# Kernel tuning notes

Hardware: AMD Instinct MI355X
Metric: run time of the kernel (lower is better)

Reference implementation:

```python
import jax, jax.numpy as jnp
import numpy as np

HIDDEN = 512
ONEHOT = 64
B, L = 128, 1024


def setup_inputs() -> dict:
    key = jax.random.key(0)
    k1, k2, k3, k4, k5 = jax.random.split(key, 5)
    hidden = jax.random.normal(k1, (B, HIDDEN), dtype=jnp.float32)
    encoder_outputs = jax.random.normal(k2, (L, B, HIDDEN + ONEHOT), dtype=jnp.float32)
    # nn.Linear(2*hidden+onehot, hidden): weight (out, in), bias (out,)
    fan_in = 2 * HIDDEN + ONEHOT
    bound = 1.0 / np.sqrt(fan_in)
    W = jax.random.uniform(k3, (HIDDEN, fan_in), minval=-bound, maxval=bound, dtype=jnp.float32)
    b = jax.random.uniform(k4, (HIDDEN,), minval=-bound, maxval=bound, dtype=jnp.float32)
    stdv = 1.0 / np.sqrt(HIDDEN)
    v = jax.random.normal(k5, (HIDDEN,), dtype=jnp.float32) * stdv
    return {"hidden": hidden, "encoder_outputs": encoder_outputs, "W": W, "b": b, "v": v}


def reference(hidden, encoder_outputs, W, b, v):
    # hidden: (B, H), encoder_outputs: (L, B, H+onehot)
    h_dim = hidden.shape[1]
    enc = jnp.transpose(encoder_outputs, (1, 0, 2))  # (B, L, H+onehot)
    # Split the linear into two partial matmuls to avoid the explicit repeat+concat:
    # attn(cat([H_rep, enc])) == hidden @ Wh.T (broadcast over L) + enc @ We.T + b
    Wh = W[:, :h_dim]          # (H, H)
    We = W[:, h_dim:]          # (H, H+onehot)
    part_h = hidden @ Wh.T      # (B, H)
    part_e = jnp.einsum('bld,hd->blh', enc, We)  # (B, L, H)
    energy = jnp.tanh(part_e + part_h[:, None, :] + b)  # (B, L, H)
    scores = jnp.einsum('blh,h->bl', energy, v)          # (B, L)
    return jax.nn.softmax(scores, axis=1)[:, None, :]    # (B, 1, L)
```

## Files before the change

### kernel.cpp

```cpp
#include <hip/hip_runtime.h>
#include <stdint.h>

#define HIDDEN 512
#define ONEHOT 64
#define EDIM   576
#define BATCH  128
#define LSEQ   1024
#define FANIN  1088

typedef __attribute__((ext_vector_type(8))) short short8;
typedef __attribute__((ext_vector_type(4))) float f32x4;

__device__ inline unsigned short f2bf(float x) {
    union { float f; unsigned int u; } v; v.f = x;
    unsigned int u = v.u;
    unsigned int r = (u + 0x7FFFu + ((u >> 16) & 1u)) >> 16;
    return (unsigned short)r;
}

__device__ inline float fast_tanh(float x) {
    float ax = fabsf(x);
    float e  = __expf(2.f * ax);
    float t  = 1.f - __fdividef(2.f, e + 1.f);
    return copysignf(t, x);
}

__global__ __launch_bounds__(256) void k_prep(const float* __restrict__ hidden,
                                              const float* __restrict__ W,
                                              const float* __restrict__ bias,
                                              float* __restrict__ ph,
                                              unsigned short* __restrict__ WeB) {
    int bid = blockIdx.x;
    int tid = threadIdx.x;
    if (bid < 256) {
        int gid = bid * 256 + tid;
        int b = gid & (BATCH - 1);
        int h = gid >> 7;
        const float* hrow = hidden + b * HIDDEN;
        const float* wrow = W + h * FANIN;
        float acc = 0.f;
#pragma unroll 4
        for (int d = 0; d < HIDDEN; d += 4) {
            float4 hv = *(const float4*)(hrow + d);
            float4 wv = *(const float4*)(wrow + d);
            acc += hv.x * wv.x + hv.y * wv.y + hv.z * wv.z + hv.w * wv.w;
        }
        ph[b * HIDDEN + h] = acc + bias[h];
    } else {
        int i = (bid - 256) * 256 + tid;
        int kc = i >> 15;
        int h  = (i >> 6) & 511;
        int g  = (i >> 3) & 7;
        int j  = i & 7;
        int k  = ((g ^ (h & 7)) << 3) | j;
        WeB[i] = f2bf(W[h * FANIN + HIDDEN + kc * 64 + k]);
    }
}

#define AROW 72

__global__ __launch_bounds__(1024, 4) void k_main(
        const float* __restrict__ enc,
        const unsigned short* __restrict__ WeB,
        const float* __restrict__ ph,
        const float* __restrict__ v,
        float* __restrict__ scoresP)
{
    __shared__ unsigned short aLds[128 * AROW];
    __shared__ unsigned short bLds[256 * 64];

    const int tid  = threadIdx.x;
    const int wave = tid >> 6;
    const int lane = tid & 63;
    const int c  = lane & 15;
    const int q  = lane >> 4;
    const int vm = wave & 3;
    const int vn = wave >> 2;

    const int id    = blockIdx.x;
    const int l     = (id & 7) * 128 + (id >> 4);
    const int ht    = (id >> 3) & 1;
    const int hbase = ht * 256;

    f32x4 acc[2][4];
#pragma unroll
    for (int i = 0; i < 2; ++i)
#pragma unroll
        for (int j = 0; j < 4; ++j) acc[i][j] = (f32x4){0.f, 0.f, 0.f, 0.f};

    const float* abase = enc + (size_t)l * (BATCH * EDIM);
    const char*  bsrc  = (const char*)WeB + (size_t)ht * 32768;

    const int row0 = tid >> 4;
    const int c4   = tid & 15;
    const float* ap0 = abase + (size_t)row0 * EDIM + c4 * 4;
    const float* ap1 = ap0 + (size_t)64 * EDIM;
    unsigned short* aw0 = &aLds[row0 * AROW + c4 * 4];
    unsigned short* aw1 = &aLds[(row0 + 64) * AROW + c4 * 4];

    for (int kc = 0; kc < 9; ++kc) {
        float4 av0 = *(const float4*)(ap0 + kc * 64);
        float4 av1 = *(const float4*)(ap1 + kc * 64);

        __syncthreads();

#pragma unroll
        for (int p = 0; p < 2; ++p) {
            int off = p * 16384 + wave * 1024 + lane * 16;
            __builtin_amdgcn_global_load_lds(
                (const __attribute__((address_space(1))) unsigned int*)
                    (bsrc + (size_t)kc * 65536 + off),
                (__attribute__((address_space(3))) unsigned int*)
                    ((char*)bLds + off),
                16, 0, 0);
        }

        {
            ushort4 w;
            w.x = f2bf(av0.x); w.y = f2bf(av0.y);
            w.z = f2bf(av0.z); w.w = f2bf(av0.w);
            *(ushort4*)aw0 = w;
            w.x = f2bf(av1.x); w.y = f2bf(av1.y);
            w.z = f2bf(av1.z); w.w = f2bf(av1.w);
            *(ushort4*)aw1 = w;
        }

        __syncthreads();

#pragma unroll
        for (int kk = 0; kk < 2; ++kk) {
            short8 af[2], bf[4];
#pragma unroll
            for (int am = 0; am < 2; ++am)
                af[am] = *(const short8*)(&aLds[(vm * 32 + am * 16 + c) * AROW + kk * 32 + q * 8]);
#pragma unroll
            for (int an = 0; an < 4; ++an) {
                int row = vn * 64 + an * 16 + c;
                int g   = ((kk << 2) | q) ^ (c & 7);
                bf[an]  = *(const short8*)((const char*)bLds + row * 128 + g * 16);
            }
#pragma unroll
            for (int am = 0; am < 2; ++am)
#pragma unroll
                for (int an = 0; an < 4; ++an)
                    acc[am][an] = __builtin_amdgcn_mfma_f32_16x16x32_bf16(
                        af[am], bf[an], acc[am][an], 0, 0, 0);
        }
    }

    float vv[4];
#pragma unroll
    for (int an = 0; an < 4; ++an) vv[an] = v[hbase + vn * 64 + an * 16 + c];

    const int slot = ht * 4 + vn;
#pragma unroll
    for (int am = 0; am < 2; ++am) {
#pragma unroll
        for (int r = 0; r < 4; ++r) {
            int b = vm * 32 + am * 16 + q * 4 + r;
            const float* phr = ph + b * HIDDEN + hbase + vn * 64 + c;
            float s = 0.f;
#pragma unroll
            for (int an = 0; an < 4; ++an) {
                float e = acc[am][an][r] + phr[an * 16];
                s += vv[an] * fast_tanh(e);
            }
            s += __shfl_xor(s, 1);
            s += __shfl_xor(s, 2);
            s += __shfl_xor(s, 4);
            s += __shfl_xor(s, 8);
            if (c == 0)
                scoresP[((size_t)slot * LSEQ + l) * BATCH + b] = s;
        }
    }
}

__global__ __launch_bounds__(256) void k_softmax(const float* __restrict__ sp,
                                                 float* __restrict__ out) {
    __shared__ float red[4];
    int b = blockIdx.x;
    int tid = threadIdx.x;
    float vals[4];
#pragma unroll
    for (int i = 0; i < 4; ++i) {
        int li = tid + i * 256;
        float s = 0.f;
#pragma unroll
        for (int sl = 0; sl < 8; ++sl)
            s += sp[((size_t)sl * LSEQ + li) * BATCH + b];
        vals[i] = s;
    }

    float m = fmaxf(fmaxf(vals[0], vals[1]), fmaxf(vals[2], vals[3]));
    for (int off = 1; off < 64; off <<= 1) m = fmaxf(m, __shfl_xor(m, off));
    int wv = tid >> 6;
    if ((tid & 63) == 0) red[wv] = m;
    __syncthreads();
    m = fmaxf(fmaxf(red[0], red[1]), fmaxf(red[2], red[3]));
    __syncthreads();

    float sum = 0.f;
#pragma unroll
    for (int i = 0; i < 4; ++i) { vals[i] = __expf(vals[i] - m); sum += vals[i]; }
    for (int off = 1; off < 64; off <<= 1) sum += __shfl_xor(sum, off);
    if ((tid & 63) == 0) red[wv] = sum;
    __syncthreads();
    sum = red[0] + red[1] + red[2] + red[3];
    float inv = 1.f / sum;
#pragma unroll
    for (int i = 0; i < 4; ++i)
        out[(size_t)b * LSEQ + tid + i * 256] = vals[i] * inv;
}

extern "C" void kernel_launch(void* const* d_in, const int* in_sizes, int n_in,
                              void* d_out, int out_size, void* d_ws, size_t ws_size,
                              hipStream_t stream) {
    const float* hidden = (const float*)d_in[0];
    const float* enc    = (const float*)d_in[1];
    const float* W      = (const float*)d_in[2];
    const float* bias   = (const float*)d_in[3];
    const float* v      = (const float*)d_in[4];
    float* out = (float*)d_out;

    char* ws = (char*)d_ws;
    float* ph           = (float*)ws;
    unsigned short* WeB = (unsigned short*)(ws + 262144);
    float* scoresP      = (float*)(ws + 851968);

    hipLaunchKernelGGL(k_prep, dim3(1408), dim3(256), 0, stream,
                       hidden, W, bias, ph, WeB);
    hipLaunchKernelGGL(k_main, dim3(2048), dim3(1024), 0, stream,
                       enc, WeB, ph, v, scoresP);
    hipLaunchKernelGGL(k_softmax, dim3(128), dim3(256), 0, stream, scoresP, out);
}
```

Measured before the change: 526.7 us.

## Double-buffer weight tiles and prefetch next K chunk in attention GEMM

The main kernel now double-buffers the LDS weight tile and prefetches the next K-chunk of encoder rows and weights while the current chunk is being computed. Explicit vmcnt/lgkmcnt waits and raw barriers replace the two __syncthreads per iteration. The partial scores layout is transposed so the softmax reads contiguous L values, and the prep dot loop is unrolled further. The extra 32 KB of LDS may lower occupancy, and the hand-written waitcnt counts risk races if the compiler reorders or adds memory operations.

```diff
diff --git a/kernel.cpp b/kernel.cpp
--- a/kernel.cpp
+++ b/kernel.cpp
@@ -39,7 +39,7 @@
         const float* hrow = hidden + b * HIDDEN;
         const float* wrow = W + h * FANIN;
         float acc = 0.f;
-#pragma unroll 4
+#pragma unroll 8
         for (int d = 0; d < HIDDEN; d += 4) {
             float4 hv = *(const float4*)(hrow + d);
             float4 wv = *(const float4*)(wrow + d);
@@ -67,7 +67,7 @@
         float* __restrict__ scoresP)
 {
     __shared__ unsigned short aLds[128 * AROW];
-    __shared__ unsigned short bLds[256 * 64];
+    __shared__ unsigned short bLds[2][256 * 64];
 
     const int tid  = threadIdx.x;
     const int wave = tid >> 6;
@@ -98,22 +98,22 @@
     unsigned short* aw0 = &aLds[row0 * AROW + c4 * 4];
     unsigned short* aw1 = &aLds[(row0 + 64) * AROW + c4 * 4];
 
+    float4 av0 = *(const float4*)(ap0);
+    float4 av1 = *(const float4*)(ap1);
+#pragma unroll
+    for (int p = 0; p < 2; ++p) {
+        int off = p * 16384 + wave * 1024 + lane * 16;
+        __builtin_amdgcn_global_load_lds(
+            (const __attribute__((address_space(1))) unsigned int*)(bsrc + off),
+            (__attribute__((address_space(3))) unsigned int*)
+                ((char*)bLds[0] + off),
+            16, 0, 0);
+    }
+
+#pragma unroll
     for (int kc = 0; kc < 9; ++kc) {
-        float4 av0 = *(const float4*)(ap0 + kc * 64);
-        float4 av1 = *(const float4*)(ap1 + kc * 64);
-
-        __syncthreads();
-
-#pragma unroll
-        for (int p = 0; p < 2; ++p) {
-            int off = p * 16384 + wave * 1024 + lane * 16;
-            __builtin_amdgcn_global_load_lds(
-                (const __attribute__((address_space(1))) unsigned int*)
-                    (bsrc + (size_t)kc * 65536 + off),
-                (__attribute__((address_space(3))) unsigned int*)
-                    ((char*)bLds + off),
-                16, 0, 0);
-        }
+        const int cur = kc & 1;
+        const int nxt = cur ^ 1;
 
         {
             ushort4 w;
@@ -125,7 +125,26 @@
             *(ushort4*)aw1 = w;
         }
 
-        __syncthreads();
+        if (kc < 8) {
+            av0 = *(const float4*)(ap0 + (kc + 1) * 64);
+            av1 = *(const float4*)(ap1 + (kc + 1) * 64);
+#pragma unroll
+            for (int p = 0; p < 2; ++p) {
+                int off = p * 16384 + wave * 1024 + lane * 16;
+                __builtin_amdgcn_global_load_lds(
+                    (const __attribute__((address_space(1))) unsigned int*)
+                        (bsrc + (size_t)(kc + 1) * 65536 + off),
+                    (__attribute__((address_space(3))) unsigned int*)
+                        ((char*)bLds[nxt] + off),
+                    16, 0, 0);
+            }
+            asm volatile("s_waitcnt vmcnt(4)" ::: "memory");
+        } else {
+            asm volatile("s_waitcnt vmcnt(0)" ::: "memory");
+        }
+        asm volatile("s_waitcnt lgkmcnt(0)" ::: "memory");
+        __builtin_amdgcn_sched_barrier(0);
+        asm volatile("s_barrier" ::: "memory");
 
 #pragma unroll
         for (int kk = 0; kk < 2; ++kk) {
@@ -137,7 +156,7 @@
             for (int an = 0; an < 4; ++an) {
                 int row = vn * 64 + an * 16 + c;
                 int g   = ((kk << 2) | q) ^ (c & 7);
-                bf[an]  = *(const short8*)((const char*)bLds + row * 128 + g * 16);
+                bf[an]  = *(const short8*)((const char*)bLds[cur] + row * 128 + g * 16);
             }
 #pragma unroll
             for (int am = 0; am < 2; ++am)
@@ -146,6 +165,9 @@
                     acc[am][an] = __builtin_amdgcn_mfma_f32_16x16x32_bf16(
                         af[am], bf[an], acc[am][an], 0, 0, 0);
         }
+
+        if (kc < 8)
+            asm volatile("s_barrier" ::: "memory");
     }
 
     float vv[4];
@@ -170,7 +192,7 @@
             s += __shfl_xor(s, 4);
             s += __shfl_xor(s, 8);
             if (c == 0)
-                scoresP[((size_t)slot * LSEQ + l) * BATCH + b] = s;
+                scoresP[((size_t)slot * BATCH + b) * LSEQ + l] = s;
         }
     }
 }
@@ -187,7 +209,7 @@
         float s = 0.f;
 #pragma unroll
         for (int sl = 0; sl < 8; ++sl)
-            s += sp[((size_t)sl * LSEQ + li) * BATCH + b];
+            s += sp[((size_t)sl * BATCH + b) * LSEQ + li];
         vals[i] = s;
     }
 
```

Result: slower. 552.0 us (+4.8%).

## Double-buffer main GEMM with larger 256x256 tiles and phased MFMA scheduling

Applied to the files above, without the earlier changes.

Reworks the main kernel so each workgroup of 512 threads computes a 256-row tile covering two sequence positions, not 128 rows of one. A and B tiles are double-buffered in dynamic LDS, and the next chunk's loads are issued while MFMA phases run, with setprio around the compute. The goal is to hide global load latency and to reuse each B tile across twice as many rows. It also changes the score layout to be contiguous along L so the softmax reads coalesce. Costs are more accumulator registers (128 floats per thread), lower occupancy and extra barriers.

```diff
diff --git a/kernel.cpp b/kernel.cpp
--- a/kernel.cpp
+++ b/kernel.cpp
@@ -39,7 +39,7 @@
         const float* hrow = hidden + b * HIDDEN;
         const float* wrow = W + h * FANIN;
         float acc = 0.f;
-#pragma unroll 4
+#pragma unroll 8
         for (int d = 0; d < HIDDEN; d += 4) {
             float4 hv = *(const float4*)(hrow + d);
             float4 wv = *(const float4*)(wrow + d);
@@ -58,121 +58,176 @@
 }
 
 #define AROW 72
-
-__global__ __launch_bounds__(1024, 4) void k_main(
+#define ABUF (256 * AROW)
+#define ABYTES (2 * ABUF * 2)
+#define BBUF 32768
+#define LDS_TOTAL (ABYTES + 2 * BBUF)
+
+__global__ __launch_bounds__(512, 2) void k_main(
         const float* __restrict__ enc,
         const unsigned short* __restrict__ WeB,
         const float* __restrict__ ph,
         const float* __restrict__ v,
         float* __restrict__ scoresP)
 {
-    __shared__ unsigned short aLds[128 * AROW];
-    __shared__ unsigned short bLds[256 * 64];
+    extern __shared__ __align__(16) char smem[];
+    unsigned short* aLds = (unsigned short*)smem;
+    char* bLdsB = smem + ABYTES;
 
     const int tid  = threadIdx.x;
     const int wave = tid >> 6;
     const int lane = tid & 63;
     const int c  = lane & 15;
     const int q  = lane >> 4;
-    const int vm = wave & 3;
-    const int vn = wave >> 2;
-
-    const int id    = blockIdx.x;
-    const int l     = (id & 7) * 128 + (id >> 4);
-    const int ht    = (id >> 3) & 1;
-    const int hbase = ht * 256;
-
-    f32x4 acc[2][4];
-#pragma unroll
-    for (int i = 0; i < 2; ++i)
+    const int wr = wave >> 2;
+    const int wc = wave & 3;
+
+    const int id  = blockIdx.x;
+    const int xcd = id & 7;
+    const int sq_ = id >> 3;
+    const int nt  = sq_ & 1;
+    const int mt  = (sq_ >> 1) + 64 * xcd;
+    const int l0  = mt * 2;
+    const int hbase = nt * 256;
+
+    f32x4 acc[8][4];
+#pragma unroll
+    for (int i = 0; i < 8; ++i)
 #pragma unroll
         for (int j = 0; j < 4; ++j) acc[i][j] = (f32x4){0.f, 0.f, 0.f, 0.f};
 
-    const float* abase = enc + (size_t)l * (BATCH * EDIM);
-    const char*  bsrc  = (const char*)WeB + (size_t)ht * 32768;
-
-    const int row0 = tid >> 4;
-    const int c4   = tid & 15;
-    const float* ap0 = abase + (size_t)row0 * EDIM + c4 * 4;
-    const float* ap1 = ap0 + (size_t)64 * EDIM;
-    unsigned short* aw0 = &aLds[row0 * AROW + c4 * 4];
-    unsigned short* aw1 = &aLds[(row0 + 64) * AROW + c4 * 4];
+    const float* abase = enc + (size_t)l0 * (BATCH * EDIM);
+    const char*  bsrc  = (const char*)WeB + nt * 32768;
+
+    const int r0 = tid >> 4;
+    const int c4 = tid & 15;
+    const float* aptr = abase + (size_t)r0 * EDIM + c4 * 4;
+    unsigned short* awbase = aLds + r0 * AROW + c4 * 4;
+
+    float4 av[8];
+
+#define STAGE_ISSUE(KOFF, NXT) do {                                           \
+    const float* asrc_ = aptr + (KOFF) * 64;                                  \
+    _Pragma("unroll")                                                         \
+    for (int fi = 0; fi < 8; ++fi)                                            \
+        av[fi] = *(const float4*)(asrc_ + (size_t)fi * 32 * EDIM);            \
+    const char* bs_ = bsrc + (size_t)(KOFF) * 65536;                          \
+    char* bd_ = bLdsB + (NXT) * BBUF;                                         \
+    _Pragma("unroll")                                                         \
+    for (int rr = 0; rr < 4; ++rr) {                                          \
+        int off_ = rr * 8192 + wave * 1024 + lane * 16;                       \
+        __builtin_amdgcn_global_load_lds(                                     \
+            (const __attribute__((address_space(1))) unsigned int*)(bs_ + off_), \
+            (__attribute__((address_space(3))) unsigned int*)(bd_ + off_),    \
+            16, 0, 0);                                                        \
+    }                                                                         \
+} while (0)
+
+#define CVT_WRITE(NXT) do {                                                   \
+    unsigned short* ad_ = awbase + (NXT) * ABUF;                              \
+    _Pragma("unroll")                                                         \
+    for (int fi = 0; fi < 8; ++fi) {                                          \
+        ushort4 w_;                                                           \
+        w_.x = f2bf(av[fi].x); w_.y = f2bf(av[fi].y);                         \
+        w_.z = f2bf(av[fi].z); w_.w = f2bf(av[fi].w);                         \
+        *(ushort4*)(ad_ + fi * 32 * AROW) = w_;                               \
+    }                                                                         \
+} while (0)
+
+#define LOAD_AFRAGS(MQ, KK)                                                   \
+    _Pragma("unroll")                                                         \
+    for (int i = 0; i < 4; ++i)                                               \
+        af[i] = *(const short8*)(aC + (size_t)(wr * 128 + ((MQ)*4 + i) * 16 + c) * AROW + (KK) * 32 + q * 8);
+
+#define LOAD_BFRAGS(KK) do {                                                  \
+    const int g_ = (((KK) << 2) | q) ^ (c & 7);                               \
+    _Pragma("unroll")                                                         \
+    for (int j = 0; j < 4; ++j)                                               \
+        bf[j] = *(const short8*)(bC + (wc * 64 + j * 16 + c) * 128 + g_ * 16); \
+} while (0)
+
+#define PHASE_COMPUTE(MQ) do {                                                \
+    __builtin_amdgcn_s_setprio(1);                                            \
+    _Pragma("unroll")                                                         \
+    for (int i = 0; i < 4; ++i)                                               \
+        _Pragma("unroll")                                                     \
+        for (int j = 0; j < 4; ++j)                                           \
+            acc[(MQ)*4 + i][j] = __builtin_amdgcn_mfma_f32_16x16x32_bf16(     \
+                af[i], bf[j], acc[(MQ)*4 + i][j], 0, 0, 0);                   \
+    __builtin_amdgcn_s_setprio(0);                                            \
+} while (0)
+
+    STAGE_ISSUE(0, 0);
+    asm volatile("s_waitcnt vmcnt(4)" ::: "memory");
+    CVT_WRITE(0);
+    __syncthreads();
 
     for (int kc = 0; kc < 9; ++kc) {
-        float4 av0 = *(const float4*)(ap0 + kc * 64);
-        float4 av1 = *(const float4*)(ap1 + kc * 64);
-
-        __syncthreads();
-
-#pragma unroll
-        for (int p = 0; p < 2; ++p) {
-            int off = p * 16384 + wave * 1024 + lane * 16;
-            __builtin_amdgcn_global_load_lds(
-                (const __attribute__((address_space(1))) unsigned int*)
-                    (bsrc + (size_t)kc * 65536 + off),
-                (__attribute__((address_space(3))) unsigned int*)
-                    ((char*)bLds + off),
-                16, 0, 0);
+        const int cur = kc & 1;
+        const int nxt = cur ^ 1;
+        const unsigned short* aC = aLds + cur * ABUF;
+        const char* bC = bLdsB + cur * BBUF;
+        short8 af[4], bf[4];
+
+        LOAD_BFRAGS(0);
+        LOAD_AFRAGS(0, 0);
+        if (kc < 8) STAGE_ISSUE(kc + 1, nxt);
+        __builtin_amdgcn_s_barrier();
+        PHASE_COMPUTE(0);
+        __builtin_amdgcn_s_barrier();
+
+        LOAD_AFRAGS(1, 0);
+        __builtin_amdgcn_s_barrier();
+        PHASE_COMPUTE(1);
+        __builtin_amdgcn_s_barrier();
+
+        LOAD_BFRAGS(1);
+        LOAD_AFRAGS(0, 1);
+        __builtin_amdgcn_s_barrier();
+        PHASE_COMPUTE(0);
+        __builtin_amdgcn_s_barrier();
+
+        LOAD_AFRAGS(1, 1);
+        if (kc < 8) {
+            asm volatile("s_waitcnt vmcnt(4)" ::: "memory");
+            CVT_WRITE(nxt);
+            __syncthreads();
         }
-
-        {
-            ushort4 w;
-            w.x = f2bf(av0.x); w.y = f2bf(av0.y);
-            w.z = f2bf(av0.z); w.w = f2bf(av0.w);
-            *(ushort4*)aw0 = w;
-            w.x = f2bf(av1.x); w.y = f2bf(av1.y);
-            w.z = f2bf(av1.z); w.w = f2bf(av1.w);
-            *(ushort4*)aw1 = w;
-        }
-
-        __syncthreads();
-
-#pragma unroll
-        for (int kk = 0; kk < 2; ++kk) {
-            short8 af[2], bf[4];
-#pragma unroll
-            for (int am = 0; am < 2; ++am)
-                af[am] = *(const short8*)(&aLds[(vm * 32 + am * 16 + c) * AROW + kk * 32 + q * 8]);
-#pragma unroll
-            for (int an = 0; an < 4; ++an) {
-                int row = vn * 64 + an * 16 + c;
-                int g   = ((kk << 2) | q) ^ (c & 7);
-                bf[an]  = *(const short8*)((const char*)bLds + row * 128 + g * 16);
-            }
-#pragma unroll
-            for (int am = 0; am < 2; ++am)
-#pragma unroll
-                for (int an = 0; an < 4; ++an)
-                    acc[am][an] = __builtin_amdgcn_mfma_f32_16x16x32_bf16(
-                        af[am], bf[an], acc[am][an], 0, 0, 0);
-        }
+        PHASE_COMPUTE(1);
     }
 
     float vv[4];
 #pragma unroll
-    for (int an = 0; an < 4; ++an) vv[an] = v[hbase + vn * 64 + an * 16 + c];
-
-    const int slot = ht * 4 + vn;
-#pragma unroll
-    for (int am = 0; am < 2; ++am) {
-#pragma unroll
-        for (int r = 0; r < 4; ++r) {
-            int b = vm * 32 + am * 16 + q * 4 + r;
-            const float* phr = ph + b * HIDDEN + hbase + vn * 64 + c;
+    for (int j = 0; j < 4; ++j) vv[j] = v[hbase + wc * 64 + j * 16 + c];
+
+    const int slot = nt * 4 + wc;
+#pragma unroll
+    for (int mb = 0; mb < 8; ++mb) {
+#pragma unroll
+        for (int rr = 0; rr < 4; ++rr) {
+            int row = wr * 128 + mb * 16 + q * 4 + rr;
+            int b   = row & 127;
+            int ll  = l0 + (row >> 7);
+            const float* phr = ph + b * HIDDEN + hbase + wc * 64 + c;
             float s = 0.f;
 #pragma unroll
-            for (int an = 0; an < 4; ++an) {
-                float e = acc[am][an][r] + phr[an * 16];
-                s += vv[an] * fast_tanh(e);
+            for (int j = 0; j < 4; ++j) {
+                float e = acc[mb][j][rr] + phr[j * 16];
+                s += vv[j] * fast_tanh(e);
             }
             s += __shfl_xor(s, 1);
             s += __shfl_xor(s, 2);
             s += __shfl_xor(s, 4);
             s += __shfl_xor(s, 8);
             if (c == 0)
-                scoresP[((size_t)slot * LSEQ + l) * BATCH + b] = s;
+                scoresP[((size_t)slot * BATCH + b) * LSEQ + ll] = s;
         }
     }
+#undef STAGE_ISSUE
+#undef CVT_WRITE
+#undef LOAD_AFRAGS
+#undef LOAD_BFRAGS
+#undef PHASE_COMPUTE
 }
 
 __global__ __launch_bounds__(256) void k_softmax(const float* __restrict__ sp,
@@ -187,7 +242,7 @@
         float s = 0.f;
 #pragma unroll
         for (int sl = 0; sl < 8; ++sl)
-            s += sp[((size_t)sl * LSEQ + li) * BATCH + b];
+            s += sp[((size_t)sl * BATCH + b) * LSEQ + li];
         vals[i] = s;
     }
 
@@ -221,15 +276,19 @@
     const float* bias   = (const float*)d_in[3];
     const float* v      = (const float*)d_in[4];
     float* out = (float*)d_out;
+    (void)ws_size;
 
     char* ws = (char*)d_ws;
     float* ph           = (float*)ws;
     unsigned short* WeB = (unsigned short*)(ws + 262144);
     float* scoresP      = (float*)(ws + 851968);
 
+    hipFuncSetAttribute((const void*)k_main,
+                        hipFuncAttributeMaxDynamicSharedMemorySize, LDS_TOTAL);
+
     hipLaunchKernelGGL(k_prep, dim3(1408), dim3(256), 0, stream,
                        hidden, W, bias, ph, WeB);
-    hipLaunchKernelGGL(k_main, dim3(2048), dim3(1024), 0, stream,
+    hipLaunchKernelGGL(k_main, dim3(1024), dim3(512), LDS_TOTAL, stream,
                        enc, WeB, ph, v, scoresP);
     hipLaunchKernelGGL(k_softmax, dim3(128), dim3(256), 0, stream, scoresP, out);
 }
```

Result: slower. 555.2 us (+5.4%).
